# Kernel tuning notes

Measured on AMD Instinct MI355X. Metric: run time of the kernel, lower is better.

Reference implementation:

```python
import jax, jax.numpy as jnp
import numpy as np

D_MODEL = 512
NUM_HEADS = 8


def setup_inputs() -> dict:
    key = jax.random.key(0)
    ks = jax.random.split(key, 12)
    B, S, D = 2, 4096, D_MODEL
    scale = 1.0 / np.sqrt(D)
    inp = {
        "q": jax.random.normal(ks[0], (B, S, D), jnp.float32),
        "k": jax.random.normal(ks[1], (B, S, D), jnp.float32),
        "v": jax.random.normal(ks[2], (B, S, D), jnp.float32),
        "w_q": jax.random.normal(ks[3], (D, D), jnp.float32) * scale,
        "b_q": jax.random.normal(ks[4], (D,), jnp.float32) * scale,
        "w_k": jax.random.normal(ks[5], (D, D), jnp.float32) * scale,
        "b_k": jax.random.normal(ks[6], (D,), jnp.float32) * scale,
        "w_v": jax.random.normal(ks[7], (D, D), jnp.float32) * scale,
        "b_v": jax.random.normal(ks[8], (D,), jnp.float32) * scale,
        "w_o": jax.random.normal(ks[9], (D, D), jnp.float32) * scale,
        "b_o": jax.random.normal(ks[10], (D,), jnp.float32) * scale,
    }
    return inp


def _split_heads(x, h):
    b, s, d = x.shape
    return x.reshape(b, s, h, d // h).transpose(0, 2, 1, 3)  # [B,H,S,dk]


def reference(q, k, v, w_q, b_q, w_k, b_k, w_v, b_v, w_o, b_o):
    h = NUM_HEADS
    # Linear projections (torch Linear: x @ W.T + b)
    qh = _split_heads(q @ w_q.T + b_q, h)
    kh = _split_heads(k @ w_k.T + b_k, h)
    vh = _split_heads(v @ w_v.T + b_v, h)
    d_k = kh.shape[-1]
    scores = jnp.einsum("bhsd,bhtd->bhst", qh, kh) / jnp.sqrt(jnp.float32(d_k))
    attn = jax.nn.softmax(scores, axis=-1)  # [B,H,S,S] - materialized, as in source
    out = jnp.einsum("bhst,bhtd->bhsd", attn, vh)
    b, _, s, dk = out.shape
    out = out.transpose(0, 2, 1, 3).reshape(b, s, h * dk)
    return out @ w_o.T + b_o
```

## Files before the change

### kernel.cpp

```cpp
#include <hip/hip_runtime.h>
#include <hip/hip_bf16.h>

#define D_MODEL 512
#define NHEAD   8
#define DK      64
#define SEQ     4096
#define BATCH   2
#define NTOK    (BATCH * SEQ)

typedef __bf16 bf16;
typedef __bf16 bf16x2 __attribute__((ext_vector_type(2)));
typedef __bf16 bf16x4 __attribute__((ext_vector_type(4)));
typedef __bf16 bf16x8 __attribute__((ext_vector_type(8)));
typedef float  f32x4  __attribute__((ext_vector_type(4)));
typedef float  f32x16 __attribute__((ext_vector_type(16)));
typedef unsigned u32x4 __attribute__((ext_vector_type(4)));
typedef unsigned int u32;

#define MFMA16(a, b, c) __builtin_amdgcn_mfma_f32_16x16x32_bf16((a), (b), (c), 0, 0, 0)
#define MFMA32(a, b, c) __builtin_amdgcn_mfma_f32_32x32x16_bf16((a), (b), (c), 0, 0, 0)

#define QSCALE 0.18033688f

__device__ __forceinline__ void gll16(const bf16* g, bf16* l) {
    __builtin_amdgcn_global_load_lds(
        (const __attribute__((address_space(1))) u32*)g,
        (__attribute__((address_space(3))) u32*)l,
        16, 0, 0);
}

__device__ __forceinline__ unsigned pkbf16(float a, float b) {
    bf16x2 t = {(bf16)a, (bf16)b};
    return __builtin_bit_cast(unsigned, t);
}

__device__ __forceinline__ void softmax_pack(const f32x16& sc, float& l,
                                             u32x4& pa, u32x4& pb) {
    float p0 = __builtin_amdgcn_exp2f(sc[0]);
    float p1 = __builtin_amdgcn_exp2f(sc[1]);
    float p2 = __builtin_amdgcn_exp2f(sc[2]);
    float p3 = __builtin_amdgcn_exp2f(sc[3]);
    l += (p0 + p1) + (p2 + p3);
    unsigned y0 = pkbf16(p0, p1), y1 = pkbf16(p2, p3);
    p0 = __builtin_amdgcn_exp2f(sc[4]);
    p1 = __builtin_amdgcn_exp2f(sc[5]);
    p2 = __builtin_amdgcn_exp2f(sc[6]);
    p3 = __builtin_amdgcn_exp2f(sc[7]);
    l += (p0 + p1) + (p2 + p3);
    unsigned y2 = pkbf16(p0, p1), y3 = pkbf16(p2, p3);
    auto s0 = __builtin_amdgcn_permlane32_swap(y0, y2, false, false);
    auto s1 = __builtin_amdgcn_permlane32_swap(y1, y3, false, false);
    pa[0] = s0[0]; pa[2] = s0[1]; pa[1] = s1[0]; pa[3] = s1[1];

    p0 = __builtin_amdgcn_exp2f(sc[8]);
    p1 = __builtin_amdgcn_exp2f(sc[9]);
    p2 = __builtin_amdgcn_exp2f(sc[10]);
    p3 = __builtin_amdgcn_exp2f(sc[11]);
    l += (p0 + p1) + (p2 + p3);
    y0 = pkbf16(p0, p1); y1 = pkbf16(p2, p3);
    p0 = __builtin_amdgcn_exp2f(sc[12]);
    p1 = __builtin_amdgcn_exp2f(sc[13]);
    p2 = __builtin_amdgcn_exp2f(sc[14]);
    p3 = __builtin_amdgcn_exp2f(sc[15]);
    l += (p0 + p1) + (p2 + p3);
    y2 = pkbf16(p0, p1); y3 = pkbf16(p2, p3);
    auto s2 = __builtin_amdgcn_permlane32_swap(y0, y2, false, false);
    auto s3 = __builtin_amdgcn_permlane32_swap(y1, y3, false, false);
    pb[0] = s2[0]; pb[2] = s2[1]; pb[1] = s3[0]; pb[3] = s3[1];
}

__global__ __launch_bounds__(256) void cvt_w(
    const float* __restrict__ wq, const float* __restrict__ wk,
    const float* __restrict__ wv, const float* __restrict__ wo,
    bf16* __restrict__ Wb)
{
    int i = blockIdx.x * 256 + threadIdx.x;
    int m = i >> 16;
    int g = i & 65535;
    const float* src = (m == 0) ? wq : (m == 1) ? wk : (m == 2) ? wv : wo;
    float4 x = *(const float4*)(src + (size_t)g * 4);
    bf16x4 y = {(bf16)x.x, (bf16)x.y, (bf16)x.z, (bf16)x.w};
    *(bf16x4*)(Wb + (size_t)m * D_MODEL * D_MODEL + (size_t)g * 4) = y;
}

__global__ __launch_bounds__(256) void cvt_x(
    const float* __restrict__ q, const float* __restrict__ k,
    const float* __restrict__ v, bf16* __restrict__ Xb)
{
    int z = blockIdx.y;
    int i = blockIdx.x * 256 + threadIdx.x;
    const float* src = (z == 0) ? q : (z == 1) ? k : v;
    float4 x = *(const float4*)(src + (size_t)i * 4);
    bf16x4 y = {(bf16)x.x, (bf16)x.y, (bf16)x.z, (bf16)x.w};
    *(bf16x4*)(Xb + (size_t)z * NTOK * D_MODEL + (size_t)i * 4) = y;
}

__global__ __launch_bounds__(256, 3) void proj_qkv(
    const bf16* __restrict__ Xb, const bf16* __restrict__ Wb,
    const float* __restrict__ bq, const float* __restrict__ bk, const float* __restrict__ bv,
    bf16* __restrict__ Qh, bf16* __restrict__ Kh, bf16* __restrict__ Vt)
{
    const int p = blockIdx.z;
    const bf16* X = Xb + (size_t)p * NTOK * D_MODEL;
    const bf16* W = Wb + (size_t)p * D_MODEL * D_MODEL;
    const float* bias = (p == 0) ? bq : (p == 1) ? bk : bv;

    __shared__ union __align__(16) {
        struct { bf16 A[128 * 64]; bf16 B[128 * 64]; } g;
        bf16 T[128][136];
    } sm;

    const int m0   = blockIdx.x * 128;
    const int n0   = blockIdx.y * 128;
    const int tid  = threadIdx.x;
    const int lane = tid & 63;
    const int wave = tid >> 6;
    const int low4 = lane & 15;
    const int quad = lane >> 4;
    const int wm   = wave >> 1;
    const int wn   = wave & 1;

    f32x4 acc[4][4];
#pragma unroll
    for (int i = 0; i < 4; ++i)
#pragma unroll
        for (int j = 0; j < 4; ++j)
            acc[i][j] = f32x4{0.f, 0.f, 0.f, 0.f};

    for (int k0 = 0; k0 < D_MODEL; k0 += 64) {
#pragma unroll
        for (int ps = 0; ps < 4; ++ps) {
            int s   = ps * 256 + tid;
            int row = s >> 3;
            int c   = (s & 7) * 8;
            bf16* la = sm.g.A + (size_t)(ps * 256 + wave * 64) * 8;
            bf16* lb = sm.g.B + (size_t)(ps * 256 + wave * 64) * 8;
            gll16(X + (size_t)(m0 + row) * D_MODEL + k0 + c, la);
            gll16(W + (size_t)(n0 + row) * D_MODEL + k0 + c, lb);
        }
        __syncthreads();

#pragma unroll
        for (int ks = 0; ks < 2; ++ks) {
            bf16x8 a[4], b[4];
#pragma unroll
            for (int i = 0; i < 4; ++i)
                a[i] = *(const bf16x8*)&sm.g.A[(size_t)(wm * 64 + i * 16 + low4) * 64 + ks * 32 + quad * 8];
#pragma unroll
            for (int j = 0; j < 4; ++j)
                b[j] = *(const bf16x8*)&sm.g.B[(size_t)(wn * 64 + j * 16 + low4) * 64 + ks * 32 + quad * 8];
#pragma unroll
            for (int i = 0; i < 4; ++i)
#pragma unroll
                for (int j = 0; j < 4; ++j)
                    acc[i][j] = MFMA16(a[i], b[j], acc[i][j]);
        }
        __syncthreads();
    }

    if (p < 2) {
        bf16* Out = (p == 0) ? Qh : Kh;
        const float sc = (p == 0) ? QSCALE : 1.0f;
#pragma unroll
        for (int j = 0; j < 4; ++j) {
            int col = n0 + wn * 64 + j * 16 + low4;
            float bcol = bias[col];
#pragma unroll
            for (int i = 0; i < 4; ++i)
#pragma unroll
                for (int r = 0; r < 4; ++r) {
                    int row = m0 + wm * 64 + i * 16 + quad * 4 + r;
                    Out[(size_t)row * D_MODEL + col] = (bf16)((acc[i][j][r] + bcol) * sc);
                }
        }
    } else {
#pragma unroll
        for (int j = 0; j < 4; ++j) {
            int col = n0 + wn * 64 + j * 16 + low4;
            float bcol = bias[col];
#pragma unroll
            for (int i = 0; i < 4; ++i)
#pragma unroll
                for (int r = 0; r < 4; ++r)
                    sm.T[wn * 64 + j * 16 + low4][wm * 64 + i * 16 + quad * 4 + r] =
                        (bf16)(acc[i][j][r] + bcol);
        }
        __syncthreads();
        const int bb = m0 >> 12;
        const int s0 = (m0 & 4095);
#pragma unroll
        for (int it = 0; it < 8; ++it) {
            int cc = it * 16 + (tid >> 4);
            int ml = (tid & 15) * 8;
            int col = n0 + cc;
            int hh = col >> 6, dd = col & 63;
            *(bf16x8*)&Vt[(((size_t)(bb * NHEAD + hh) * DK + dd) << 12) + s0 + ml] =
                *(const bf16x8*)&sm.T[cc][ml];
        }
    }
}

__global__ __launch_bounds__(512, 2) void attn(
    const bf16* __restrict__ Qh, const bf16* __restrict__ Kh,
    const bf16* __restrict__ Vt, bf16* __restrict__ O)
{
    __shared__ union __align__(16) {
        struct { bf16 Ks[2][128][72]; bf16 Vs[2][64][136]; } s;
        float Obuf[4][32][68];
    } sm;
    __shared__ float Lbuf[4][32];

    const int q0   = blockIdx.x * 256;
    const int bh   = blockIdx.y;
    const int b    = bh >> 3, h = bh & 7;
    const int tid  = threadIdx.x;
    const int lane = tid & 63;
    const int wave = tid >> 6;
    const int qg   = wave >> 1;
    const int kg   = wave & 1;
    const int m32  = lane & 31;
    const int hl   = lane >> 5;

    const bf16* Kbase = Kh + (size_t)b * SEQ * D_MODEL + h * DK;
    const bf16* Vbase = Vt + (size_t)bh * DK * SEQ;

    const bf16* Qrow0 = Qh + (size_t)(b * SEQ + q0 + qg * 64 + m32) * D_MODEL + h * DK;
    const bf16* Qrow1 = Qrow0 + (size_t)32 * D_MODEL;
    bf16x8 qf0[4], qf1[4];
#pragma unroll
    for (int ks = 0; ks < 4; ++ks) {
        qf0[ks] = *(const bf16x8*)(Qrow0 + ks * 16 + hl * 8);
        qf1[ks] = *(const bf16x8*)(Qrow1 + ks * 16 + hl * 8);
    }

    float l0 = 0.f, l1 = 0.f;
    f32x16 acc00, acc01, acc10, acc11;
#pragma unroll
    for (int i = 0; i < 16; ++i) {
        acc00[i] = 0.f; acc01[i] = 0.f; acc10[i] = 0.f; acc11[i] = 0.f;
    }

    int kr[2], kc[2], vr[2], vc[2];
#pragma unroll
    for (int it = 0; it < 2; ++it) {
        int c = tid + it * 512;
        kr[it] = c >> 3;  kc[it] = (c & 7) * 8;
        vr[it] = c >> 4;  vc[it] = (c & 15) * 8;
    }
    bf16x8 gk[2], gv[2];
#pragma unroll
    for (int it = 0; it < 2; ++it) {
        gk[it] = *(const bf16x8*)(Kbase + (size_t)kr[it] * D_MODEL + kc[it]);
        gv[it] = *(const bf16x8*)(Vbase + (size_t)vr[it] * SEQ + vc[it]);
    }
#pragma unroll
    for (int it = 0; it < 2; ++it) {
        *(bf16x8*)&sm.s.Ks[0][kr[it]][kc[it]] = gk[it];
        *(bf16x8*)&sm.s.Vs[0][vr[it]][vc[it]] = gv[it];
    }

    for (int t0 = 0; t0 < SEQ; t0 += 128) {
        const int cur = (t0 >> 7) & 1;
        const bool pf = (t0 + 128 < SEQ);

        if (pf) {
#pragma unroll
            for (int it = 0; it < 2; ++it) {
                gk[it] = *(const bf16x8*)(Kbase + (size_t)(t0 + 128 + kr[it]) * D_MODEL + kc[it]);
                gv[it] = *(const bf16x8*)(Vbase + (size_t)vr[it] * SEQ + t0 + 128 + vc[it]);
            }
        }

        __syncthreads();

        u32x4 pq0[4], pq1[4];
#pragma unroll
        for (int mt = 0; mt < 2; ++mt) {
            f32x16 s0, s1;
#pragma unroll
            for (int i = 0; i < 16; ++i) { s0[i] = 0.f; s1[i] = 0.f; }
            __builtin_amdgcn_s_setprio(1);
#pragma unroll
            for (int ks = 0; ks < 4; ++ks) {
                bf16x8 kf = *(const bf16x8*)&sm.s.Ks[cur][kg * 64 + mt * 32 + m32][ks * 16 + hl * 8];
                s0 = MFMA32(kf, qf0[ks], s0);
                s1 = MFMA32(kf, qf1[ks], s1);
            }
            __builtin_amdgcn_s_setprio(0);
            u32x4 a0, b0, a1, b1;
            softmax_pack(s0, l0, a0, b0);
            softmax_pack(s1, l1, a1, b1);
            pq0[2 * mt] = a0; pq0[2 * mt + 1] = b0;
            pq1[2 * mt] = a1; pq1[2 * mt + 1] = b1;
        }

        __builtin_amdgcn_s_setprio(1);
#pragma unroll
        for (int ksl = 0; ksl < 4; ++ksl) {
            bf16x8 pA = __builtin_bit_cast(bf16x8, pq0[ksl]);
            bf16x8 pB = __builtin_bit_cast(bf16x8, pq1[ksl]);
            bf16x8 v0 = *(const bf16x8*)&sm.s.Vs[cur][0 * 32 + m32][kg * 64 + ksl * 16 + hl * 8];
            acc00 = MFMA32(pA, v0, acc00);
            acc10 = MFMA32(pB, v0, acc10);
            bf16x8 v1 = *(const bf16x8*)&sm.s.Vs[cur][1 * 32 + m32][kg * 64 + ksl * 16 + hl * 8];
            acc01 = MFMA32(pA, v1, acc01);
            acc11 = MFMA32(pB, v1, acc11);
        }
        __builtin_amdgcn_s_setprio(0);

        if (pf) {
#pragma unroll
            for (int it = 0; it < 2; ++it) {
                *(bf16x8*)&sm.s.Ks[cur ^ 1][kr[it]][kc[it]] = gk[it];
                *(bf16x8*)&sm.s.Vs[cur ^ 1][vr[it]][vc[it]] = gv[it];
            }
        }
    }

    l0 += __shfl_xor(l0, 32);
    l1 += __shfl_xor(l1, 32);

#pragma unroll
    for (int qs = 0; qs < 2; ++qs) {
        float l = (qs == 0) ? l0 : l1;
        __syncthreads();
        if (kg == 1) {
#pragma unroll
            for (int r = 0; r < 16; ++r) {
                int qq = (r & 3) + 8 * (r >> 2) + 4 * hl;
                sm.Obuf[qg][qq][0 * 32 + m32] = (qs == 0) ? acc00[r] : acc10[r];
                sm.Obuf[qg][qq][1 * 32 + m32] = (qs == 0) ? acc01[r] : acc11[r];
            }
            if (hl == 0) Lbuf[qg][m32] = l;
        }
        __syncthreads();
        if (kg == 0) {
            float lt  = l + Lbuf[qg][m32];
            float inv = 1.0f / lt;
#pragma unroll
            for (int r = 0; r < 16; ++r) {
                int qq = (r & 3) + 8 * (r >> 2) + 4 * hl;
                float v0 = ((qs == 0) ? acc00[r] : acc10[r]) + sm.Obuf[qg][qq][0 * 32 + m32];
                float v1 = ((qs == 0) ? acc01[r] : acc11[r]) + sm.Obuf[qg][qq][1 * 32 + m32];
                float iv = __shfl(inv, qq);
                size_t row = (size_t)(b * SEQ + q0 + qg * 64 + qs * 32 + qq);
                O[row * D_MODEL + h * DK + 0 * 32 + m32] = (bf16)(v0 * iv);
                O[row * D_MODEL + h * DK + 1 * 32 + m32] = (bf16)(v1 * iv);
            }
        }
    }
}

__global__ __launch_bounds__(256, 4) void proj_out(
    const bf16* __restrict__ Oin, const bf16* __restrict__ Wo,
    const float* __restrict__ bo, float* __restrict__ out)
{
    __shared__ __align__(16) bf16 As[64 * 64];
    __shared__ __align__(16) bf16 Bs[128 * 64];

    const int m0   = blockIdx.x * 64;
    const int n0   = blockIdx.y * 128;
    const int tid  = threadIdx.x;
    const int lane = tid & 63;
    const int wave = tid >> 6;
    const int low4 = lane & 15;
    const int quad = lane >> 4;
    const int wm   = wave >> 1;
    const int wn   = wave & 1;

    f32x4 acc[2][4];
#pragma unroll
    for (int i = 0; i < 2; ++i)
#pragma unroll
        for (int j = 0; j < 4; ++j)
            acc[i][j] = f32x4{0.f, 0.f, 0.f, 0.f};

    for (int k0 = 0; k0 < D_MODEL; k0 += 64) {
#pragma unroll
        for (int ps = 0; ps < 2; ++ps) {
            int s   = ps * 256 + tid;
            int row = s >> 3;
            int c   = (s & 7) * 8;
            bf16* la = As + (size_t)(ps * 256 + wave * 64) * 8;
            gll16(Oin + (size_t)(m0 + row) * D_MODEL + k0 + c, la);
        }
#pragma unroll
        for (int ps = 0; ps < 4; ++ps) {
            int s   = ps * 256 + tid;
            int row = s >> 3;
            int c   = (s & 7) * 8;
            bf16* lb = Bs + (size_t)(ps * 256 + wave * 64) * 8;
            gll16(Wo + (size_t)(n0 + row) * D_MODEL + k0 + c, lb);
        }
        __syncthreads();

#pragma unroll
        for (int ks = 0; ks < 2; ++ks) {
            bf16x8 a[2], b[4];
#pragma unroll
            for (int i = 0; i < 2; ++i)
                a[i] = *(const bf16x8*)&As[(size_t)(wm * 32 + i * 16 + low4) * 64 + ks * 32 + quad * 8];
#pragma unroll
            for (int j = 0; j < 4; ++j)
                b[j] = *(const bf16x8*)&Bs[(size_t)(wn * 64 + j * 16 + low4) * 64 + ks * 32 + quad * 8];
#pragma unroll
            for (int i = 0; i < 2; ++i)
#pragma unroll
                for (int j = 0; j < 4; ++j)
                    acc[i][j] = MFMA16(a[i], b[j], acc[i][j]);
        }
        __syncthreads();
    }

#pragma unroll
    for (int j = 0; j < 4; ++j) {
        int col = n0 + wn * 64 + j * 16 + low4;
        float bcol = bo[col];
#pragma unroll
        for (int i = 0; i < 2; ++i)
#pragma unroll
            for (int r = 0; r < 4; ++r) {
                int row = m0 + wm * 32 + i * 16 + quad * 4 + r;
                out[(size_t)row * D_MODEL + col] = acc[i][j][r] + bcol;
            }
    }
}

extern "C" void kernel_launch(void* const* d_in, const int* in_sizes, int n_in,
                              void* d_out, int out_size, void* d_ws, size_t ws_size,
                              hipStream_t stream)
{
    const float* q  = (const float*)d_in[0];
    const float* k  = (const float*)d_in[1];
    const float* v  = (const float*)d_in[2];
    const float* wq = (const float*)d_in[3];
    const float* bq = (const float*)d_in[4];
    const float* wk = (const float*)d_in[5];
    const float* bk = (const float*)d_in[6];
    const float* wv = (const float*)d_in[7];
    const float* bv = (const float*)d_in[8];
    const float* wo = (const float*)d_in[9];
    const float* bo = (const float*)d_in[10];

    const size_t NT = (size_t)NTOK * D_MODEL;
    bf16* Qh = (bf16*)d_ws;
    bf16* Kh = Qh + NT;
    bf16* Vt = Kh + NT;
    bf16* O  = Vt + NT;
    bf16* Wb = O + NT;
    bf16* Xb = Wb + (size_t)4 * D_MODEL * D_MODEL;

    cvt_w<<<1024, 256, 0, stream>>>(wq, wk, wv, wo, Wb);

    dim3 gx(4096, 3);
    cvt_x<<<gx, 256, 0, stream>>>(q, k, v, Xb);

    dim3 g1(NTOK / 128, D_MODEL / 128, 3);
    proj_qkv<<<g1, 256, 0, stream>>>(Xb, Wb, bq, bk, bv, Qh, Kh, Vt);

    dim3 g2(SEQ / 256, BATCH * NHEAD);
    attn<<<g2, 512, 0, stream>>>(Qh, Kh, Vt, O);

    dim3 g3(NTOK / 64, D_MODEL / 128);
    proj_out<<<g3, 256, 0, stream>>>(O, Wb + (size_t)3 * D_MODEL * D_MODEL, bo, (float*)d_out);
}
```

Before: 214.0 us.

## Merge conversion kernels and halve attention block to 128 queries with 4 waves

```diff
diff --git a/kernel.cpp b/kernel.cpp
--- a/kernel.cpp
+++ b/kernel.cpp
@@ -69,30 +69,31 @@
     pb[0] = s2[0]; pb[2] = s2[1]; pb[1] = s3[0]; pb[3] = s3[1];
 }
 
-__global__ __launch_bounds__(256) void cvt_w(
+__global__ __launch_bounds__(256) void cvt_all(
     const float* __restrict__ wq, const float* __restrict__ wk,
     const float* __restrict__ wv, const float* __restrict__ wo,
-    bf16* __restrict__ Wb)
+    const float* __restrict__ q,  const float* __restrict__ k,
+    const float* __restrict__ v,
+    bf16* __restrict__ Wb, bf16* __restrict__ Xb)
 {
-    int i = blockIdx.x * 256 + threadIdx.x;
-    int m = i >> 16;
-    int g = i & 65535;
-    const float* src = (m == 0) ? wq : (m == 1) ? wk : (m == 2) ? wv : wo;
-    float4 x = *(const float4*)(src + (size_t)g * 4);
-    bf16x4 y = {(bf16)x.x, (bf16)x.y, (bf16)x.z, (bf16)x.w};
-    *(bf16x4*)(Wb + (size_t)m * D_MODEL * D_MODEL + (size_t)g * 4) = y;
-}
-
-__global__ __launch_bounds__(256) void cvt_x(
-    const float* __restrict__ q, const float* __restrict__ k,
-    const float* __restrict__ v, bf16* __restrict__ Xb)
-{
-    int z = blockIdx.y;
-    int i = blockIdx.x * 256 + threadIdx.x;
-    const float* src = (z == 0) ? q : (z == 1) ? k : v;
-    float4 x = *(const float4*)(src + (size_t)i * 4);
-    bf16x4 y = {(bf16)x.x, (bf16)x.y, (bf16)x.z, (bf16)x.w};
-    *(bf16x4*)(Xb + (size_t)z * NTOK * D_MODEL + (size_t)i * 4) = y;
+    int bid = blockIdx.x;
+    if (bid < 1024) {
+        int i = bid * 256 + threadIdx.x;
+        int m = i >> 16;
+        int g = i & 65535;
+        const float* src = (m == 0) ? wq : (m == 1) ? wk : (m == 2) ? wv : wo;
+        float4 x = *(const float4*)(src + (size_t)g * 4);
+        bf16x4 y = {(bf16)x.x, (bf16)x.y, (bf16)x.z, (bf16)x.w};
+        *(bf16x4*)(Wb + (size_t)m * D_MODEL * D_MODEL + (size_t)g * 4) = y;
+    } else {
+        int i = (bid - 1024) * 256 + threadIdx.x;
+        int z = i >> 20;
+        int g = i & 1048575;
+        const float* src = (z == 0) ? q : (z == 1) ? k : v;
+        float4 x = *(const float4*)(src + (size_t)g * 4);
+        bf16x4 y = {(bf16)x.x, (bf16)x.y, (bf16)x.z, (bf16)x.w};
+        *(bf16x4*)(Xb + (size_t)z * NTOK * D_MODEL + (size_t)g * 4) = y;
+    }
 }
 
 __global__ __launch_bounds__(256, 3) void proj_qkv(
@@ -200,17 +201,17 @@
     }
 }
 
-__global__ __launch_bounds__(512, 2) void attn(
+__global__ __launch_bounds__(256, 2) void attn(
     const bf16* __restrict__ Qh, const bf16* __restrict__ Kh,
     const bf16* __restrict__ Vt, bf16* __restrict__ O)
 {
     __shared__ union __align__(16) {
         struct { bf16 Ks[2][128][72]; bf16 Vs[2][64][136]; } s;
-        float Obuf[4][32][68];
+        float Obuf[2][32][68];
     } sm;
-    __shared__ float Lbuf[4][32];
-
-    const int q0   = blockIdx.x * 256;
+    __shared__ float Lbuf[2][32];
+
+    const int q0   = blockIdx.x * 128;
     const int bh   = blockIdx.y;
     const int b    = bh >> 3, h = bh & 7;
     const int tid  = threadIdx.x;
@@ -235,26 +236,28 @@
 
     float l0 = 0.f, l1 = 0.f;
     f32x16 acc00, acc01, acc10, acc11;
+    f32x16 ZERO;
 #pragma unroll
     for (int i = 0; i < 16; ++i) {
         acc00[i] = 0.f; acc01[i] = 0.f; acc10[i] = 0.f; acc11[i] = 0.f;
-    }
-
-    int kr[2], kc[2], vr[2], vc[2];
-#pragma unroll
-    for (int it = 0; it < 2; ++it) {
-        int c = tid + it * 512;
+        ZERO[i] = 0.f;
+    }
+
+    int kr[4], kc[4], vr[4], vc[4];
+#pragma unroll
+    for (int it = 0; it < 4; ++it) {
+        int c = tid + it * 256;
         kr[it] = c >> 3;  kc[it] = (c & 7) * 8;
         vr[it] = c >> 4;  vc[it] = (c & 15) * 8;
     }
-    bf16x8 gk[2], gv[2];
-#pragma unroll
-    for (int it = 0; it < 2; ++it) {
+    bf16x8 gk[4], gv[4];
+#pragma unroll
+    for (int it = 0; it < 4; ++it) {
         gk[it] = *(const bf16x8*)(Kbase + (size_t)kr[it] * D_MODEL + kc[it]);
         gv[it] = *(const bf16x8*)(Vbase + (size_t)vr[it] * SEQ + vc[it]);
     }
 #pragma unroll
-    for (int it = 0; it < 2; ++it) {
+    for (int it = 0; it < 4; ++it) {
         *(bf16x8*)&sm.s.Ks[0][kr[it]][kc[it]] = gk[it];
         *(bf16x8*)&sm.s.Vs[0][vr[it]][vc[it]] = gv[it];
     }
@@ -265,7 +268,7 @@
 
         if (pf) {
 #pragma unroll
-            for (int it = 0; it < 2; ++it) {
+            for (int it = 0; it < 4; ++it) {
                 gk[it] = *(const bf16x8*)(Kbase + (size_t)(t0 + 128 + kr[it]) * D_MODEL + kc[it]);
                 gv[it] = *(const bf16x8*)(Vbase + (size_t)vr[it] * SEQ + t0 + 128 + vc[it]);
             }
@@ -276,12 +279,12 @@
         u32x4 pq0[4], pq1[4];
 #pragma unroll
         for (int mt = 0; mt < 2; ++mt) {
-            f32x16 s0, s1;
-#pragma unroll
-            for (int i = 0; i < 16; ++i) { s0[i] = 0.f; s1[i] = 0.f; }
             __builtin_amdgcn_s_setprio(1);
-#pragma unroll
-            for (int ks = 0; ks < 4; ++ks) {
+            bf16x8 kf0 = *(const bf16x8*)&sm.s.Ks[cur][kg * 64 + mt * 32 + m32][0 * 16 + hl * 8];
+            f32x16 s0 = MFMA32(kf0, qf0[0], ZERO);
+            f32x16 s1 = MFMA32(kf0, qf1[0], ZERO);
+#pragma unroll
+            for (int ks = 1; ks < 4; ++ks) {
                 bf16x8 kf = *(const bf16x8*)&sm.s.Ks[cur][kg * 64 + mt * 32 + m32][ks * 16 + hl * 8];
                 s0 = MFMA32(kf, qf0[ks], s0);
                 s1 = MFMA32(kf, qf1[ks], s1);
@@ -310,7 +313,7 @@
 
         if (pf) {
 #pragma unroll
-            for (int it = 0; it < 2; ++it) {
+            for (int it = 0; it < 4; ++it) {
                 *(bf16x8*)&sm.s.Ks[cur ^ 1][kr[it]][kc[it]] = gk[it];
                 *(bf16x8*)&sm.s.Vs[cur ^ 1][vr[it]][vc[it]] = gv[it];
             }
@@ -450,16 +453,13 @@
     bf16* Wb = O + NT;
     bf16* Xb = Wb + (size_t)4 * D_MODEL * D_MODEL;
 
-    cvt_w<<<1024, 256, 0, stream>>>(wq, wk, wv, wo, Wb);
-
-    dim3 gx(4096, 3);
-    cvt_x<<<gx, 256, 0, stream>>>(q, k, v, Xb);
+    cvt_all<<<13312, 256, 0, stream>>>(wq, wk, wv, wo, q, k, v, Wb, Xb);
 
     dim3 g1(NTOK / 128, D_MODEL / 128, 3);
     proj_qkv<<<g1, 256, 0, stream>>>(Xb, Wb, bq, bk, bv, Qh, Kh, Vt);
 
-    dim3 g2(SEQ / 256, BATCH * NHEAD);
-    attn<<<g2, 512, 0, stream>>>(Qh, Kh, Vt, O);
+    dim3 g2(SEQ / 128, BATCH * NHEAD);
+    attn<<<g2, 256, 0, stream>>>(Qh, Kh, Vt, O);
 
     dim3 g3(NTOK / 64, D_MODEL / 128);
     proj_out<<<g3, 256, 0, stream>>>(O, Wb + (size_t)3 * D_MODEL * D_MODEL, bo, (float*)d_out);
```

After: 218.3 us. About the same (+2.0%).
